# Performance work log

Hardware: AMD Instinct MI355X
Metric: run time of the kernel (lower is better)

## Reference

```python
import jax, jax.numpy as jnp
import numpy as np

B, T, H, DK, DV = 4, 2048, 1024, 1024, 1024


def setup_inputs() -> dict:
    key = jax.random.key(0)
    ks = jax.random.split(key, 9)
    s = lambda fan_in: 1.0 / np.sqrt(fan_in)
    return {
        "y_all": jax.random.normal(ks[0], (B, T, H), dtype=jnp.float32),
        "Wq": jax.random.uniform(ks[1], (H, DK), jnp.float32, -s(H), s(H)),
        "bq": jax.random.uniform(ks[2], (DK,), jnp.float32, -s(H), s(H)),
        "Wk": jax.random.uniform(ks[3], (H, DK), jnp.float32, -s(H), s(H)),
        "bk": jax.random.uniform(ks[4], (DK,), jnp.float32, -s(H), s(H)),
        "Wv": jax.random.uniform(ks[5], (H, DV), jnp.float32, -s(H), s(H)),
        "bv": jax.random.uniform(ks[6], (DV,), jnp.float32, -s(H), s(H)),
        "Wo": jax.random.uniform(ks[7], (DV, H), jnp.float32, -s(DV), s(DV)),
        "bo": jax.random.uniform(ks[8], (H,), jnp.float32, -s(DV), s(DV)),
    }


def reference(y_all, Wq, bq, Wk, bk, Wv, bv, Wo, bo):
    # Fused causal attention equivalent to the per-timestep Python loop.
    dk = Wq.shape[1]
    q = (y_all @ Wq + bq) / jnp.sqrt(jnp.asarray(dk, y_all.dtype))  # [B,T,DK]
    k = y_all @ Wk + bk                                             # [B,T,DK]
    v = y_all @ Wv + bv                                             # [B,T,DV]
    scores = jnp.einsum("bqd,bkd->bqk", q, k)                       # [B,T,T]
    t = y_all.shape[1]
    causal = jnp.tril(jnp.ones((t, t), dtype=bool))                 # [T,T]
    scores = jnp.where(causal[None], scores, jnp.asarray(-jnp.inf, scores.dtype))
    w = jax.nn.softmax(scores, axis=-1)                             # [B,T,T]
    ctx = jnp.einsum("bqk,bkd->bqd", w, v)                          # [B,T,DV]
    return ctx @ Wo + bo                                            # [B,T,H]
```

## Files before the change

### kernel.cpp

```cpp
#include <hip/hip_runtime.h>
#include <hip/hip_bf16.h>
#include <cstdint>

#define DEVI __device__ __forceinline__

typedef __attribute__((ext_vector_type(8))) short bf16x8;
typedef __attribute__((ext_vector_type(4))) short bf16x4;
typedef __attribute__((ext_vector_type(4))) float f32x4;

DEVI short f2bf(float f) {
  unsigned u = __float_as_uint(f);
  u += 0x7fff + ((u >> 16) & 1);
  return (short)(u >> 16);
}
DEVI float bf2f(short s) { return __uint_as_float(((unsigned)(unsigned short)s) << 16); }

DEVI void gl_lds16(const short* g, short* l) {
  __builtin_amdgcn_global_load_lds((const __attribute__((address_space(1))) unsigned*)g,
                                   (__attribute__((address_space(3))) unsigned*)l, 16, 0, 0);
}

constexpr int BM = 128, BN = 128, BK = 64;

template<int MODE, int BIASMODE, bool OUTF32, int DECODE>
__global__ __launch_bounds__(256, 2)
void gemm_bt(const short* __restrict__ A, const short* __restrict__ B,
             void* __restrict__ Cv, const float* __restrict__ b0,
             float scale, int K, int lda, int ldb, int ldc,
             long long sA, long long sB, long long sC, int tdim)
{
  const int nwg = gridDim.x, orig = blockIdx.x;
  const int q8 = nwg >> 3, r8 = nwg & 7;
  const int xcd = orig & 7, idx8 = orig >> 3;
  const int wg = (xcd < r8 ? xcd * (q8 + 1) : r8 * (q8 + 1) + (xcd - r8) * q8) + idx8;
  const int bz = blockIdx.z;

  int bi, bj;
  if constexpr (MODE == 4) {
    int b = (int)((__fsqrt_rn(8.f * (float)wg + 1.f) - 1.f) * 0.5f);
    if ((b + 1) * (b + 2) / 2 <= wg) ++b;
    if (b * (b + 1) / 2 > wg) --b;
    bi = b; bj = wg - b * (b + 1) / 2;
  } else {
    bi = wg / tdim;
    bj = wg - bi * tdim;
    if constexpr (DECODE == 3) { if (bz & 2) bi = (nwg / tdim) - 1 - bi; }
  }

  A += (long long)bz * sA;
  B += (long long)bz * sB;

  __shared__ __align__(16) short lA[2][BM * BK];
  __shared__ __align__(16) short lB[2][BN * BK];

  const int tid = threadIdx.x, wave = tid >> 6, lane = tid & 63;
  const int wr = wave >> 1, wc = wave & 1;
  const int brow = bi * BM, bcol = bj * BN;
  const int fr = lane & 15, h = lane >> 4;

  const int ck0 = ((h ^ (fr & 7))) * 8;
  const int swc = ((tid & 7) ^ ((tid >> 3) & 7)) * 8;
  const short* pA = A + (long long)(brow + (tid >> 3)) * lda + swc;
  const short* pB = B + (long long)(bcol + (tid >> 3)) * ldb + swc;

  f32x4 acc[4][4] = {};
  const int kend = (MODE == 2) ? (bi + 1) * BM : K;
  const int nt = kend / BK;

  auto stage = [&](int buf, int t) {
    const long long ko = (long long)t * BK;
#pragma unroll
    for (int j = 0; j < 4; ++j)
      gl_lds16(pA + (long long)(j * 32) * lda + ko, &lA[buf][j * 2048 + tid * 8]);
#pragma unroll
    for (int j = 0; j < 4; ++j)
      gl_lds16(pB + (long long)(j * 32) * ldb + ko, &lB[buf][j * 2048 + tid * 8]);
  };

  stage(0, 0);
  __syncthreads();

  int cur = 0;
  for (int t = 0; t < nt; ++t) {
    if (t + 1 < nt) stage(cur ^ 1, t + 1);

    const short* bufA = lA[cur];
    const short* bufB = lB[cur];
    bf16x8 af[4], bg[4];
#pragma unroll
    for (int m = 0; m < 4; ++m)
      af[m] = *(const bf16x8*)&bufA[(wr * 64 + m * 16 + fr) * BK + ck0];
#pragma unroll
    for (int n = 0; n < 4; ++n)
      bg[n] = *(const bf16x8*)&bufB[(wc * 64 + n * 16 + fr) * BK + ck0];
#pragma unroll
    for (int m = 0; m < 4; ++m)
#pragma unroll
      for (int n = 0; n < 4; ++n)
        acc[m][n] = __builtin_amdgcn_mfma_f32_16x16x32_bf16(af[m], bg[n], acc[m][n], 0, 0, 0);
#pragma unroll
    for (int m = 0; m < 4; ++m)
      af[m] = *(const bf16x8*)&bufA[((wr * 64 + m * 16 + fr) * BK + ck0) ^ 32];
#pragma unroll
    for (int n = 0; n < 4; ++n)
      bg[n] = *(const bf16x8*)&bufB[((wc * 64 + n * 16 + fr) * BK + ck0) ^ 32];
#pragma unroll
    for (int m = 0; m < 4; ++m)
#pragma unroll
      for (int n = 0; n < 4; ++n)
        acc[m][n] = __builtin_amdgcn_mfma_f32_16x16x32_bf16(af[m], bg[n], acc[m][n], 0, 0, 0);

    __syncthreads();
    cur ^= 1;
  }

  const int lrow = h * 4;
  float* Cf = (float*)Cv + (long long)bz * sC;
  short* Cs = (short*)Cv + (long long)bz * sC;
  int colg[4]; float bvv[4];
#pragma unroll
  for (int n = 0; n < 4; ++n) {
    colg[n] = bcol + wc * 64 + n * 16 + fr;
    bvv[n] = (BIASMODE == 1) ? b0[colg[n]] : 0.f;
  }
#pragma unroll
  for (int m = 0; m < 4; ++m) {
    const int row = brow + wr * 64 + m * 16 + lrow;
#pragma unroll
    for (int j = 0; j < 4; ++j) {
#pragma unroll
      for (int n = 0; n < 4; ++n) {
        const float val = (acc[m][n][j] + bvv[n]) * scale;
        if constexpr (OUTF32) Cf[(long long)(row + j) * ldc + colg[n]] = val;
        else                  Cs[(long long)(row + j) * ldc + colg[n]] = f2bf(val);
      }
    }
  }
}

__global__ __launch_bounds__(256, 4)
void gemm_zg(const short* __restrict__ WvoT, const short* __restrict__ ybf,
             const short* __restrict__ MTb, short* __restrict__ zT,
             short* __restrict__ G, const float* __restrict__ wvec)
{
  const int orig = blockIdx.x;
  const int xcd = orig & 7, idx8 = orig >> 3;
  const int wg = xcd * 128 + idx8;

  const short *A, *B; short* C; const float* b0; float scale; int ldc, tdim, lwg;
  if (wg < 512) { A = WvoT; B = ybf; C = zT; b0 = nullptr; scale = 1.f;
                  ldc = 8192; tdim = 64; lwg = wg; }
  else          { A = ybf; B = MTb; C = G; b0 = wvec; scale = 1.f / 32.f;
                  ldc = 1024; tdim = 8; lwg = wg - 512; }
  const int bi = lwg / tdim, bj = lwg - bi * tdim;

  __shared__ __align__(16) short lA[BM * BK];
  __shared__ __align__(16) short lB[BN * BK];

  const int tid = threadIdx.x, wave = tid >> 6, lane = tid & 63;
  const int wr = wave >> 1, wc = wave & 1;
  const int brow = bi * BM, bcol = bj * BN;
  const int fr = lane & 15, h = lane >> 4;

  const int ck0 = ((h ^ (fr & 7))) * 8;
  const int swc = ((tid & 7) ^ ((tid >> 3) & 7)) * 8;
  const short* pA = A + (long long)(brow + (tid >> 3)) * 1024 + swc;
  const short* pB = B + (long long)(bcol + (tid >> 3)) * 1024 + swc;

  f32x4 acc[4][4] = {};

  for (int t = 0; t < 16; ++t) {
    const long long ko = (long long)t * BK;
#pragma unroll
    for (int j = 0; j < 4; ++j)
      gl_lds16(pA + (long long)(j * 32) * 1024 + ko, &lA[j * 2048 + tid * 8]);
#pragma unroll
    for (int j = 0; j < 4; ++j)
      gl_lds16(pB + (long long)(j * 32) * 1024 + ko, &lB[j * 2048 + tid * 8]);
    __syncthreads();

    bf16x8 af[4], bg[4];
#pragma unroll
    for (int m = 0; m < 4; ++m)
      af[m] = *(const bf16x8*)&lA[(wr * 64 + m * 16 + fr) * BK + ck0];
#pragma unroll
    for (int n = 0; n < 4; ++n)
      bg[n] = *(const bf16x8*)&lB[(wc * 64 + n * 16 + fr) * BK + ck0];
#pragma unroll
    for (int m = 0; m < 4; ++m)
#pragma unroll
      for (int n = 0; n < 4; ++n)
        acc[m][n] = __builtin_amdgcn_mfma_f32_16x16x32_bf16(af[m], bg[n], acc[m][n], 0, 0, 0);
#pragma unroll
    for (int m = 0; m < 4; ++m)
      af[m] = *(const bf16x8*)&lA[((wr * 64 + m * 16 + fr) * BK + ck0) ^ 32];
#pragma unroll
    for (int n = 0; n < 4; ++n)
      bg[n] = *(const bf16x8*)&lB[((wc * 64 + n * 16 + fr) * BK + ck0) ^ 32];
#pragma unroll
    for (int m = 0; m < 4; ++m)
#pragma unroll
      for (int n = 0; n < 4; ++n)
        acc[m][n] = __builtin_amdgcn_mfma_f32_16x16x32_bf16(af[m], bg[n], acc[m][n], 0, 0, 0);
    __syncthreads();
  }

  const int lrow = h * 4;
  int colg[4]; float bvv[4];
#pragma unroll
  for (int n = 0; n < 4; ++n) {
    colg[n] = bcol + wc * 64 + n * 16 + fr;
    bvv[n] = b0 ? b0[colg[n]] : 0.f;
  }
#pragma unroll
  for (int m = 0; m < 4; ++m) {
    const int row = brow + wr * 64 + m * 16 + lrow;
#pragma unroll
    for (int j = 0; j < 4; ++j) {
#pragma unroll
      for (int n = 0; n < 4; ++n)
        C[(long long)(row + j) * ldc + colg[n]] = f2bf((acc[m][n][j] + bvv[n]) * scale);
    }
  }
}

__global__ __launch_bounds__(256)
void softmax_causal_bf16_k(short* __restrict__ sc)
{
  const int T = 2048;
  const long long row = blockIdx.x;
  const int t = (int)(row & (T - 1));
  short* ps = sc + row * (long long)T;
  const int tid = threadIdx.x, wave = tid >> 6, lane = tid & 63;
  const int c0 = tid * 8;
  const int wlim = ((t >> 7) + 1) << 7;

  bf16x8 v = {};
  if (c0 <= t) v = *(const bf16x8*)&ps[c0];
  float x[8];
#pragma unroll
  for (int j = 0; j < 8; ++j) x[j] = bf2f(v[j]);

  float mx = -3.0e38f;
#pragma unroll
  for (int j = 0; j < 8; ++j) if (c0 + j <= t) mx = fmaxf(mx, x[j]);
#pragma unroll
  for (int o = 32; o; o >>= 1) mx = fmaxf(mx, __shfl_xor(mx, o, 64));
  __shared__ float red[8];
  if (lane == 0) red[wave] = mx;
  __syncthreads();
  const float M = fmaxf(fmaxf(red[0], red[1]), fmaxf(red[2], red[3]));

  float e[8], s = 0.f;
#pragma unroll
  for (int j = 0; j < 8; ++j) { e[j] = (c0 + j <= t) ? __expf(x[j] - M) : 0.f; s += e[j]; }
#pragma unroll
  for (int o = 32; o; o >>= 1) s += __shfl_xor(s, o, 64);
  if (lane == 0) red[4 + wave] = s;
  __syncthreads();
  const float inv = 1.f / (red[4] + red[5] + red[6] + red[7]);

  if (c0 < wlim) {
    bf16x8 ov;
#pragma unroll
    for (int j = 0; j < 8; ++j) ov[j] = f2bf(e[j] * inv);
    *(bf16x8*)&ps[c0] = ov;
  }
}

__global__ __launch_bounds__(256)
void cvt_y_k(const float* __restrict__ y, short* __restrict__ ybf)
{
  const long long i = (long long)blockIdx.x * 256 + threadIdx.x;
  const float4 v0 = ((const float4*)y)[i * 2];
  const float4 v1 = ((const float4*)y)[i * 2 + 1];
  bf16x8 o;
  o[0] = f2bf(v0.x); o[1] = f2bf(v0.y); o[2] = f2bf(v0.z); o[3] = f2bf(v0.w);
  o[4] = f2bf(v1.x); o[5] = f2bf(v1.y); o[6] = f2bf(v1.z); o[7] = f2bf(v1.w);
  ((bf16x8*)ybf)[i] = o;
}

__global__ __launch_bounds__(256)
void cvt_w_all_k(const float* __restrict__ w0, const float* __restrict__ w1,
                 const float* __restrict__ w2, const float* __restrict__ w3,
                 short* __restrict__ o0, short* __restrict__ o1,
                 short* __restrict__ o2, short* __restrict__ o3)
{
  const int tx = threadIdx.x & 31, ty = threadIdx.x >> 5;
  const int r0 = blockIdx.y * 32, c0 = blockIdx.x * 32;
  if (blockIdx.z != 2) {
    const float* in = (blockIdx.z == 0) ? w0 : (blockIdx.z == 1 ? w1 : w3);
    short* out      = (blockIdx.z == 0) ? o0 : (blockIdx.z == 1 ? o1 : o3);
#pragma unroll
    for (int i = 0; i < 4; ++i)
      out[(long long)(r0 + ty + 8 * i) * 1024 + c0 + tx] =
          f2bf(in[(long long)(r0 + ty + 8 * i) * 1024 + c0 + tx]);
    return;
  }
  __shared__ float tile[32][33];
#pragma unroll
  for (int i = 0; i < 4; ++i)
    tile[ty + 8 * i][tx] = w2[(long long)(r0 + ty + 8 * i) * 1024 + c0 + tx];
  __syncthreads();
#pragma unroll
  for (int i = 0; i < 4; ++i)
    o2[(long long)(c0 + ty + 8 * i) * 1024 + r0 + tx] = f2bf(tile[tx][ty + 8 * i]);
}

__global__ __launch_bounds__(256)
void bias_init_k(const float* __restrict__ bo, float* __restrict__ outb)
{
  const int j = blockIdx.x * 256 + threadIdx.x;
  outb[j] = bo[j];
}

__global__ __launch_bounds__(256)
void bias_fold_k(const float* __restrict__ bv, const float* __restrict__ Wo,
                 float* __restrict__ outb)
{
  const int r0 = blockIdx.x * 16;
  const int c4 = threadIdx.x;
  float4 acc = make_float4(0.f, 0.f, 0.f, 0.f);
  for (int r = 0; r < 16; ++r) {
    const float s = bv[r0 + r];
    const float4 w = ((const float4*)(Wo + (long long)(r0 + r) * 1024))[c4];
    acc.x += s * w.x; acc.y += s * w.y; acc.z += s * w.z; acc.w += s * w.w;
  }
  atomicAdd(&outb[c4 * 4 + 0], acc.x);
  atomicAdd(&outb[c4 * 4 + 1], acc.y);
  atomicAdd(&outb[c4 * 4 + 2], acc.z);
  atomicAdd(&outb[c4 * 4 + 3], acc.w);
}

__global__ __launch_bounds__(256)
void wkbq_gemv_k(const float* __restrict__ Wk, const float* __restrict__ bq,
                 float* __restrict__ w)
{
  const int row = blockIdx.x, tid = threadIdx.x;
  const float4 a = ((const float4*)(Wk + (long long)row * 1024))[tid];
  const float4 b = ((const float4*)bq)[tid];
  float s = a.x * b.x + a.y * b.y + a.z * b.z + a.w * b.w;
#pragma unroll
  for (int o = 32; o; o >>= 1) s += __shfl_xor(s, o, 64);
  __shared__ float red[4];
  if ((tid & 63) == 0) red[tid >> 6] = s;
  __syncthreads();
  if (tid == 0) w[row] = red[0] + red[1] + red[2] + red[3];
}

__global__ __launch_bounds__(256)
void combine4_k(const float* __restrict__ p, short* __restrict__ out)
{
  const long long i = (long long)blockIdx.x * 256 + threadIdx.x;
  const float4 a = ((const float4*)p)[i];
  const float4 b = ((const float4*)(p + 1048576))[i];
  const float4 c = ((const float4*)(p + 2097152))[i];
  const float4 d = ((const float4*)(p + 3145728))[i];
  bf16x4 o;
  o[0] = f2bf(a.x + b.x + c.x + d.x);
  o[1] = f2bf(a.y + b.y + c.y + d.y);
  o[2] = f2bf(a.z + b.z + c.z + d.z);
  o[3] = f2bf(a.w + b.w + c.w + d.w);
  ((bf16x4*)out)[i] = o;
}

extern "C" void kernel_launch(void* const* d_in, const int* in_sizes, int n_in,
                              void* d_out, int out_size, void* d_ws, size_t ws_size,
                              hipStream_t stream)
{
  (void)in_sizes; (void)n_in; (void)out_size; (void)ws_size;
  const float* y  = (const float*)d_in[0];
  const float* Wq = (const float*)d_in[1];
  const float* bq = (const float*)d_in[2];
  const float* Wk = (const float*)d_in[3];
  const float* bk = (const float*)d_in[4];
  const float* Wv = (const float*)d_in[5];
  const float* bv = (const float*)d_in[6];
  const float* Wo = (const float*)d_in[7];
  const float* bo = (const float*)d_in[8];
  float* out = (float*)d_out;
  (void)bk;

  const int T = 2048;
  const long long MT = 8192;
  const long long MM = 1048576;

  short* ws    = (short*)d_ws;
  short* ybf   = ws;
  short* WqBf  = ybf + MT * 1024;
  short* WkBf  = WqBf + MM;
  short* WoT   = WkBf + MM;
  short* WvBf  = WoT + MM;
  short* MTb   = WvBf + MM;
  short* WvoT  = MTb + MM;
  short* G     = WvoT + MM;
  short* zT    = G + MT * 1024;
  short* scores = zT + MT * 1024;
  float* bvWoBo = (float*)(scores + 4ll * T * T);
  float* wvec   = bvWoBo + 1024;
  float* part   = wvec + 1024;

  cvt_y_k<<<4096, 256, 0, stream>>>(y, ybf);
  cvt_w_all_k<<<dim3(32, 32, 4), 256, 0, stream>>>(
      Wq, Wk, Wo, Wv, WqBf, WkBf, WoT, WvBf);
  bias_init_k<<<4, 256, 0, stream>>>(bo, bvWoBo);
  bias_fold_k<<<64, 256, 0, stream>>>(bv, Wo, bvWoBo);
  wkbq_gemv_k<<<1024, 256, 0, stream>>>(Wk, bq, wvec);

  gemm_bt<0, 0, true, 0><<<dim3(64, 1, 4), 256, 0, stream>>>(
      WoT, WvBf, part, nullptr, 1.f, 256, 1024, 1024, 1024,
      256, 256, 1048576, 8);
  combine4_k<<<1024, 256, 0, stream>>>(part, WvoT);

  gemm_bt<0, 0, true, 0><<<dim3(64, 1, 4), 256, 0, stream>>>(
      WkBf, WqBf, part, nullptr, 1.f, 256, 1024, 1024, 1024,
      256, 256, 1048576, 8);
  combine4_k<<<1024, 256, 0, stream>>>(part, MTb);

  gemm_zg<<<1024, 256, 0, stream>>>(WvoT, ybf, MTb, zT, G, wvec);

  gemm_bt<4, 0, false, 0><<<dim3(136, 1, 4), 256, 0, stream>>>(
      G, ybf, scores, nullptr, 1.f, 1024, 1024, 1024, T,
      (long long)T * 1024, (long long)T * 1024, (long long)T * T, 16);

  softmax_causal_bf16_k<<<(int)MT, 256, 0, stream>>>(scores);

  gemm_bt<2, 1, true, 3><<<dim3(16 * 8, 1, 4), 256, 0, stream>>>(
      scores, zT, out, bvWoBo, 1.f, T, T, 8192, 1024,
      (long long)T * T, 2048, 2048ll * 1024, 8);
}
```

Measured before the change: 186.1 us.

## Regroup GEMM launches: compute G alone, then fuse causal scores with zT GEMM

The combined zT+G launch is split. G is now computed in its own kernel, and the zT projection GEMM is merged with the causal scores GEMM into one launch of 1056 blocks. Lower-triangular tiles are mapped from a flat index through a sqrt-based triangular decode. The aim is to fill the GPU better by pairing the independent zT work with the scores tiles, which depend on G, so neither leaves a poorly occupied launch. The scores path no longer goes through the generic gemm_bt kernel, and the two weight-precombine GEMMs are reordered.

```diff
diff --git a/kernel.cpp b/kernel.cpp
--- a/kernel.cpp
+++ b/kernel.cpp
@@ -139,20 +139,13 @@
 }
 
 __global__ __launch_bounds__(256, 4)
-void gemm_zg(const short* __restrict__ WvoT, const short* __restrict__ ybf,
-             const short* __restrict__ MTb, short* __restrict__ zT,
-             short* __restrict__ G, const float* __restrict__ wvec)
+void gemm_g(const short* __restrict__ ybf, const short* __restrict__ MTb,
+            short* __restrict__ G, const float* __restrict__ wvec)
 {
   const int orig = blockIdx.x;
   const int xcd = orig & 7, idx8 = orig >> 3;
-  const int wg = xcd * 128 + idx8;
-
-  const short *A, *B; short* C; const float* b0; float scale; int ldc, tdim, lwg;
-  if (wg < 512) { A = WvoT; B = ybf; C = zT; b0 = nullptr; scale = 1.f;
-                  ldc = 8192; tdim = 64; lwg = wg; }
-  else          { A = ybf; B = MTb; C = G; b0 = wvec; scale = 1.f / 32.f;
-                  ldc = 1024; tdim = 8; lwg = wg - 512; }
-  const int bi = lwg / tdim, bj = lwg - bi * tdim;
+  const int wg = xcd * 64 + idx8;
+  const int bi = wg >> 3, bj = wg & 7;
 
   __shared__ __align__(16) short lA[BM * BK];
   __shared__ __align__(16) short lB[BN * BK];
@@ -164,6 +157,102 @@
 
   const int ck0 = ((h ^ (fr & 7))) * 8;
   const int swc = ((tid & 7) ^ ((tid >> 3) & 7)) * 8;
+  const short* pA = ybf + (long long)(brow + (tid >> 3)) * 1024 + swc;
+  const short* pB = MTb + (long long)(bcol + (tid >> 3)) * 1024 + swc;
+
+  f32x4 acc[4][4] = {};
+
+  for (int t = 0; t < 16; ++t) {
+    const long long ko = (long long)t * BK;
+#pragma unroll
+    for (int j = 0; j < 4; ++j)
+      gl_lds16(pA + (long long)(j * 32) * 1024 + ko, &lA[j * 2048 + tid * 8]);
+#pragma unroll
+    for (int j = 0; j < 4; ++j)
+      gl_lds16(pB + (long long)(j * 32) * 1024 + ko, &lB[j * 2048 + tid * 8]);
+    __syncthreads();
+
+    bf16x8 af[4], bg[4];
+#pragma unroll
+    for (int m = 0; m < 4; ++m)
+      af[m] = *(const bf16x8*)&lA[(wr * 64 + m * 16 + fr) * BK + ck0];
+#pragma unroll
+    for (int n = 0; n < 4; ++n)
+      bg[n] = *(const bf16x8*)&lB[(wc * 64 + n * 16 + fr) * BK + ck0];
+#pragma unroll
+    for (int m = 0; m < 4; ++m)
+#pragma unroll
+      for (int n = 0; n < 4; ++n)
+        acc[m][n] = __builtin_amdgcn_mfma_f32_16x16x32_bf16(af[m], bg[n], acc[m][n], 0, 0, 0);
+#pragma unroll
+    for (int m = 0; m < 4; ++m)
+      af[m] = *(const bf16x8*)&lA[((wr * 64 + m * 16 + fr) * BK + ck0) ^ 32];
+#pragma unroll
+    for (int n = 0; n < 4; ++n)
+      bg[n] = *(const bf16x8*)&lB[((wc * 64 + n * 16 + fr) * BK + ck0) ^ 32];
+#pragma unroll
+    for (int m = 0; m < 4; ++m)
+#pragma unroll
+      for (int n = 0; n < 4; ++n)
+        acc[m][n] = __builtin_amdgcn_mfma_f32_16x16x32_bf16(af[m], bg[n], acc[m][n], 0, 0, 0);
+    __syncthreads();
+  }
+
+  const int lrow = h * 4;
+  int colg[4]; float bvv[4];
+#pragma unroll
+  for (int n = 0; n < 4; ++n) {
+    colg[n] = bcol + wc * 64 + n * 16 + fr;
+    bvv[n] = wvec[colg[n]];
+  }
+#pragma unroll
+  for (int m = 0; m < 4; ++m) {
+    const int row = brow + wr * 64 + m * 16 + lrow;
+#pragma unroll
+    for (int j = 0; j < 4; ++j)
+#pragma unroll
+      for (int n = 0; n < 4; ++n)
+        G[(long long)(row + j) * 1024 + colg[n]] =
+            f2bf((acc[m][n][j] + bvv[n]) * (1.f / 32.f));
+  }
+}
+
+__global__ __launch_bounds__(256, 4)
+void gemm_sz(const short* __restrict__ G, const short* __restrict__ ybf,
+             const short* __restrict__ WvoT, short* __restrict__ scores,
+             short* __restrict__ zT)
+{
+  const int orig = blockIdx.x;
+  const int xcd = orig & 7, idx8 = orig >> 3;
+  const int wg = xcd * 132 + idx8;
+
+  const short *A, *B; short* C; int ldc, bi, bj;
+  if (wg < 544) {
+    const int z = wg / 136, t = wg - z * 136;
+    int b = (int)((__fsqrt_rn(8.f * (float)t + 1.f) - 1.f) * 0.5f);
+    if ((b + 1) * (b + 2) / 2 <= t) ++b;
+    if (b * (b + 1) / 2 > t) --b;
+    bi = b; bj = t - b * (b + 1) / 2;
+    A = G + (long long)z * 2048 * 1024;
+    B = ybf + (long long)z * 2048 * 1024;
+    C = scores + (long long)z * 2048 * 2048;
+    ldc = 2048;
+  } else {
+    const int lwg = wg - 544;
+    bi = lwg >> 6; bj = lwg & 63;
+    A = WvoT; B = ybf; C = zT; ldc = 8192;
+  }
+
+  __shared__ __align__(16) short lA[BM * BK];
+  __shared__ __align__(16) short lB[BN * BK];
+
+  const int tid = threadIdx.x, wave = tid >> 6, lane = tid & 63;
+  const int wr = wave >> 1, wc = wave & 1;
+  const int brow = bi * BM, bcol = bj * BN;
+  const int fr = lane & 15, h = lane >> 4;
+
+  const int ck0 = ((h ^ (fr & 7))) * 8;
+  const int swc = ((tid & 7) ^ ((tid >> 3) & 7)) * 8;
   const short* pA = A + (long long)(brow + (tid >> 3)) * 1024 + swc;
   const short* pB = B + (long long)(bcol + (tid >> 3)) * 1024 + swc;
 
@@ -206,21 +295,17 @@
   }
 
   const int lrow = h * 4;
-  int colg[4]; float bvv[4];
-#pragma unroll
-  for (int n = 0; n < 4; ++n) {
-    colg[n] = bcol + wc * 64 + n * 16 + fr;
-    bvv[n] = b0 ? b0[colg[n]] : 0.f;
-  }
+  int colg[4];
+#pragma unroll
+  for (int n = 0; n < 4; ++n) colg[n] = bcol + wc * 64 + n * 16 + fr;
 #pragma unroll
   for (int m = 0; m < 4; ++m) {
     const int row = brow + wr * 64 + m * 16 + lrow;
 #pragma unroll
-    for (int j = 0; j < 4; ++j) {
-#pragma unroll
-      for (int n = 0; n < 4; ++n)
-        C[(long long)(row + j) * ldc + colg[n]] = f2bf((acc[m][n][j] + bvv[n]) * scale);
-    }
+    for (int j = 0; j < 4; ++j)
+#pragma unroll
+      for (int n = 0; n < 4; ++n)
+        C[(long long)(row + j) * ldc + colg[n]] = f2bf(acc[m][n][j]);
   }
 }
 
@@ -408,20 +493,18 @@
   wkbq_gemv_k<<<1024, 256, 0, stream>>>(Wk, bq, wvec);
 
   gemm_bt<0, 0, true, 0><<<dim3(64, 1, 4), 256, 0, stream>>>(
+      WkBf, WqBf, part, nullptr, 1.f, 256, 1024, 1024, 1024,
+      256, 256, 1048576, 8);
+  combine4_k<<<1024, 256, 0, stream>>>(part, MTb);
+
+  gemm_bt<0, 0, true, 0><<<dim3(64, 1, 4), 256, 0, stream>>>(
       WoT, WvBf, part, nullptr, 1.f, 256, 1024, 1024, 1024,
       256, 256, 1048576, 8);
   combine4_k<<<1024, 256, 0, stream>>>(part, WvoT);
 
-  gemm_bt<0, 0, true, 0><<<dim3(64, 1, 4), 256, 0, stream>>>(
-      WkBf, WqBf, part, nullptr, 1.f, 256, 1024, 1024, 1024,
-      256, 256, 1048576, 8);
-  combine4_k<<<1024, 256, 0, stream>>>(part, MTb);
-
-  gemm_zg<<<1024, 256, 0, stream>>>(WvoT, ybf, MTb, zT, G, wvec);
-
-  gemm_bt<4, 0, false, 0><<<dim3(136, 1, 4), 256, 0, stream>>>(
-      G, ybf, scores, nullptr, 1.f, 1024, 1024, 1024, T,
-      (long long)T * 1024, (long long)T * 1024, (long long)T * T, 16);
+  gemm_g<<<512, 256, 0, stream>>>(ybf, MTb, G, wvec);
+
+  gemm_sz<<<1056, 256, 0, stream>>>(G, ybf, WvoT, scores, zT);
 
   softmax_causal_bf16_k<<<(int)MT, 256, 0, stream>>>(scores);
 
```

Result: faster. 180.0 us (-3.3%).
